# Optimization experiments

Hardware: AMD Instinct MI355X
Metric: run time of the kernel (lower is better)

## Reference

```python
import jax, jax.numpy as jnp
import numpy as np

TREE_DEPTH = 8
N_INTERNAL = 2 ** TREE_DEPTH - 1   # 255
N_LEAVES = 2 ** TREE_DEPTH         # 256
N_CLASSES = 100
N_TREES = 16
BATCH = 8192
D_FEAT = 1024
TEMPERATURE = 1.0


def setup_inputs() -> dict:
    key = jax.random.key(0)
    k1, k2, k3, k4, k5 = jax.random.split(key, 5)
    x = jax.random.normal(k1, (BATCH, D_FEAT), dtype=jnp.float32)
    # scale weights ~1/sqrt(D) so split logits are O(1) (avoids sigmoid saturation)
    split_weights = jax.random.normal(k2, (N_TREES, N_INTERNAL, D_FEAT), dtype=jnp.float32) / np.sqrt(D_FEAT)
    split_bias = jax.random.normal(k3, (N_TREES, N_INTERNAL), dtype=jnp.float32)
    leaf_logits = jax.random.normal(k4, (N_TREES, N_LEAVES, N_CLASSES), dtype=jnp.float32)
    tree_weights = jax.random.normal(k5, (N_TREES,), dtype=jnp.float32)
    return {"x": x, "split_weights": split_weights, "split_bias": split_bias,
            "leaf_logits": leaf_logits, "tree_weights": tree_weights}


def reference(x, split_weights, split_bias, leaf_logits, tree_weights):
    # All internal-node split logits in one contraction: [T, B, N_INTERNAL]
    logits = jnp.einsum('bd,tnd->tbn', x, split_weights) + split_bias[:, None, :]
    split_prob = jax.nn.sigmoid(logits / TEMPERATURE)  # P(go right) per heap node
    T, B = split_prob.shape[0], split_prob.shape[1]
    # Level-order path products. Heap layout: level d occupies nodes [2^d-1, 2^(d+1)-2].
    # Child j of a node splits into (left=2j, right=2j+1) at next level -> interleave.
    mu = jnp.ones((T, B, 1), dtype=x.dtype)
    for d in range(TREE_DEPTH):
        start = 2 ** d - 1
        p = split_prob[:, :, start:start + 2 ** d]          # [T, B, 2^d]
        mu = jnp.stack([mu * (1.0 - p), mu * p], axis=-1)   # left, right
        mu = mu.reshape(T, B, 2 ** (d + 1))
    # mu: [T, B, N_LEAVES] leaf reach probabilities, ordering matches leaf_idx
    leaf_dist = jax.nn.softmax(leaf_logits, axis=-1)        # [T, L, C]
    per_tree = jnp.einsum('tbl,tlc->tbc', mu, leaf_dist)    # [T, B, C]
    w = jax.nn.softmax(tree_weights, axis=0)[:, None, None]
    return (per_tree * w).sum(axis=0)                       # [B, C]
```

## Files before the change

### kernel.cpp

```cpp
#include <hip/hip_runtime.h>
#include <hip/hip_fp16.h>

typedef _Float16 f16;
typedef _Float16 f16x4 __attribute__((ext_vector_type(4)));
typedef _Float16 f16x8 __attribute__((ext_vector_type(8)));
typedef float    f32x4 __attribute__((ext_vector_type(4)));

constexpr int TREES = 16;
constexpr int NNODE = 255;
constexpr int NCLS  = 100;
constexpr int NCPAD = 112;
constexpr int NB    = 8192;
constexpr int DF    = 1024;
constexpr int KTOT  = TREES * 256;

constexpr size_t XH_OFF = 0;
constexpr size_t WH_OFF = XH_OFF + (size_t)NB * DF;
constexpr size_t SD_OFF = WH_OFF + (size_t)TREES * 256 * DF;
constexpr size_t BP_OFF = SD_OFF + (size_t)NCPAD * KTOT;
constexpr size_t PT_OFF_F = (BP_OFF + 8192) / 2;

#define WAIT_VMCNT(n) asm volatile("s_waitcnt vmcnt(" #n ")" ::: "memory")
#define WAIT_LGKM0()  asm volatile("s_waitcnt lgkmcnt(0)" ::: "memory")
__device__ __forceinline__ void BAR() {
  asm volatile("" ::: "memory");
  __builtin_amdgcn_s_barrier();
  asm volatile("" ::: "memory");
}

__device__ __forceinline__ void gload_lds16(const f16* g, f16* l) {
  __builtin_amdgcn_global_load_lds(
      (const __attribute__((address_space(1))) void*)g,
      (__attribute__((address_space(3))) void*)l, 16, 0, 0);
}

__global__ void prep_all_k(const float* __restrict__ x, const float* __restrict__ w,
                           const float* __restrict__ ll, const float* __restrict__ twin,
                           const float* __restrict__ sb,
                           f16* __restrict__ xh, f16* __restrict__ wh,
                           f16* __restrict__ sdt, float* __restrict__ bp) {
  int bid = blockIdx.x;
  if (bid < 4096) {
    int i = bid * 256 + threadIdx.x;
    const float4* s = (const float4*)x + (size_t)i * 2;
    float4 u = s[0], v = s[1];
    f16x8 h = {(f16)u.x, (f16)u.y, (f16)u.z, (f16)u.w,
               (f16)v.x, (f16)v.y, (f16)v.z, (f16)v.w};
    *((f16x8*)xh + i) = h;
  } else if (bid < 6144) {
    int i = (bid - 4096) * 256 + threadIdx.x;
    int flat = i * 8;
    int t = flat >> 18;
    int r = (flat >> 10) & 255;
    int k = flat & 1023;
    f16x8 h;
    if (r < NNODE) {
      const float4* s = (const float4*)(w + ((size_t)(t * NNODE + r) * DF + k));
      float4 u = s[0], v = s[1];
      h = (f16x8){(f16)u.x, (f16)u.y, (f16)u.z, (f16)u.w,
                  (f16)v.x, (f16)v.y, (f16)v.z, (f16)v.w};
    } else {
      h = (f16x8){(f16)0.f, (f16)0.f, (f16)0.f, (f16)0.f,
                  (f16)0.f, (f16)0.f, (f16)0.f, (f16)0.f};
    }
    *((f16x8*)wh + i) = h;
  } else {
    int wv   = threadIdx.x >> 6;
    int lane = threadIdx.x & 63;
    int id   = (bid - 6144) * 4 + wv;
    int t    = id >> 8;
    int node = id & 255;

    float wm = -1e30f;
#pragma unroll
    for (int i = 0; i < 16; ++i) wm = fmaxf(wm, twin[i]);
    float wsum = 0.f;
#pragma unroll
    for (int i = 0; i < 16; ++i) wsum += __expf(twin[i] - wm);
    float wt = __expf(twin[t] - wm) / wsum;

    const float* rowp = ll + (size_t)id * NCLS;
    float v1 = rowp[lane];
    bool has2 = (lane + 64) < NCLS;
    float v2 = has2 ? rowp[lane + 64] : -1e30f;
    float mx = fmaxf(v1, v2);
#pragma unroll
    for (int m = 32; m; m >>= 1) mx = fmaxf(mx, __shfl_xor(mx, m, 64));
    float e1 = __expf(v1 - mx);
    float e2 = has2 ? __expf(v2 - mx) : 0.f;
    float ss = e1 + e2;
#pragma unroll
    for (int m = 32; m; m >>= 1) ss += __shfl_xor(ss, m, 64);
    float inv = wt / ss;

    sdt[(size_t)lane * KTOT + id] = (f16)(e1 * inv);
    if (lane + 64 < NCPAD)
      sdt[(size_t)(lane + 64) * KTOT + id] = has2 ? (f16)(e2 * inv) : (f16)0.f;
    if (lane == 0) bp[id] = (node < NNODE) ? sb[(size_t)t * NNODE + node] : 0.f;
  }
}

__global__ __launch_bounds__(512, 2) void tree_gemm1(
    const f16* __restrict__ xh, const f16* __restrict__ wh,
    const float* __restrict__ biasp, const f16* __restrict__ sdt,
    float* __restrict__ ptree) {
  __shared__ f16 smem[81920];
  char* smb = (char*)smem;

  const int tid  = threadIdx.x;
  const int lane = tid & 63;
  const int wid  = tid >> 6;
  const int l15  = lane & 15;
  const int lq   = lane >> 4;
  const int wrow = (wid >> 2) * 128;
  const int wcol = (wid & 3) * 64;

  int bid  = blockIdx.x;
  int xcd  = bid & 7;
  int idx  = bid >> 3;
  int t    = (xcd & 1) * 8 + (idx & 7);
  int brow = (xcd >> 1) * 8 + (idx >> 3);

  const f16* xsrc = xh + (size_t)brow * 256 * DF;
  const f16* wsrc = wh + (size_t)t * 256 * DF;

  auto stage2 = [&](int kt, int b, int pair) {
    f16* base = smem + b * 16384 + pair * 8192;
    const f16* src = (pair == 0 ? xsrc : wsrc) + kt * 32;
#pragma unroll
    for (int ch = 0; ch < 2; ++ch) {
      int u = ch * 512 + tid;
      int r = u >> 2;
      int ci = (u & 3) ^ (r & 3);
      gload_lds16(src + (size_t)r * DF + ci * 8, base + u * 8);
    }
  };

  f32x4 acc[8][4];
#pragma unroll
  for (int m = 0; m < 8; ++m)
#pragma unroll
    for (int n = 0; n < 4; ++n) acc[m][n] = (f32x4){0.f, 0.f, 0.f, 0.f};

  stage2(0, 0, 0); stage2(0, 0, 1);
  stage2(1, 1, 0); stage2(1, 1, 1);
  WAIT_VMCNT(4);
  BAR();

  for (int kt = 0; kt < 32; ++kt) {
    const char* Ab = smb + (kt % 3) * 32768;
    const char* Bb = Ab + 16384;
    const int nb3 = (kt + 2) % 3;
    f16x8 af[4], bf[4], ag[4];

#pragma unroll
    for (int m = 0; m < 4; ++m) {
      int r = wrow + m * 16 + l15;
      af[m] = *(const f16x8*)(Ab + ((r * 64 + lq * 16) ^ ((r & 3) << 4)));
    }
#pragma unroll
    for (int n = 0; n < 4; ++n) {
      int r = wcol + n * 16 + l15;
      bf[n] = *(const f16x8*)(Bb + ((r * 64 + lq * 16) ^ ((r & 3) << 4)));
    }
    if (kt < 30) stage2(kt + 2, nb3, 0);
    BAR();
    WAIT_LGKM0();
    __builtin_amdgcn_sched_barrier(0);
    __builtin_amdgcn_s_setprio(1);
#pragma unroll
    for (int m = 0; m < 4; ++m)
#pragma unroll
      for (int n = 0; n < 4; ++n)
        acc[m][n] = __builtin_amdgcn_mfma_f32_16x16x32_f16(bf[n], af[m], acc[m][n], 0, 0, 0);
    __builtin_amdgcn_s_setprio(0);
    __builtin_amdgcn_sched_barrier(0);

#pragma unroll
    for (int m = 0; m < 4; ++m) {
      int r = wrow + 64 + m * 16 + l15;
      ag[m] = *(const f16x8*)(Ab + ((r * 64 + lq * 16) ^ ((r & 3) << 4)));
    }
    if (kt < 30) stage2(kt + 2, nb3, 1);
    BAR();
    WAIT_LGKM0();
    __builtin_amdgcn_sched_barrier(0);
    __builtin_amdgcn_s_setprio(1);
#pragma unroll
    for (int m = 0; m < 4; ++m)
#pragma unroll
      for (int n = 0; n < 4; ++n)
        acc[m + 4][n] = __builtin_amdgcn_mfma_f32_16x16x32_f16(bf[n], ag[m], acc[m + 4][n], 0, 0, 0);
    __builtin_amdgcn_s_setprio(0);
    __builtin_amdgcn_sched_barrier(0);

    if (kt < 30)       { WAIT_VMCNT(4); BAR(); }
    else if (kt == 30) { WAIT_VMCNT(0); BAR(); }
  }

  char* Sb = smb;
  char* Ub = smb + 32768;
  char* Pb = smb + 98304;

  auto stage_sdt = [&](int c0, int nrows) {
    int nch = nrows * 32;
    for (int q = tid; q < nch; q += 512) {
      int rr = q >> 5;
      int jj = q & 31;
      gload_lds16(sdt + (size_t)(c0 + rr) * KTOT + t * 256 + ((jj * 8) ^ ((rr & 7) << 3)),
                  smem + q * 8);
    }
  };
  stage_sdt(0, 64);

  f16x4 ph[8][4];
#pragma unroll
  for (int m = 0; m < 8; ++m) {
#pragma unroll
    for (int n = 0; n < 4; ++n) {
      int col = wcol + n * 16 + lq * 4;
      float4 b4 = *(const float4*)(biasp + t * 256 + col);
#pragma unroll
      for (int reg = 0; reg < 4; ++reg) {
        float bv = (reg == 0) ? b4.x : (reg == 1) ? b4.y : (reg == 2) ? b4.z : b4.w;
        float z = acc[m][n][reg] + bv;
        ph[m][n][reg] = (f16)__builtin_amdgcn_rcpf(1.f + __expf(-z));
      }
    }
  }

  for (int h = 0; h < 2; ++h) {
    if ((wid >> 2) == h) {
#pragma unroll
      for (int m = 0; m < 8; ++m) {
#pragma unroll
        for (int n = 0; n < 4; ++n) {
          int r = m * 16 + l15;
          int nodeb = (wcol + n * 16 + lq * 4) * 2;
          *(f16x4*)(Pb + ((r * 512 + nodeb) ^ ((r & 7) << 4))) = ph[m][n];
        }
      }
    }
    __syncthreads();

    {
      int r = tid >> 2;
      int c = tid & 3;
      auto PRs = [&](int node) -> float {
        return (float)*(const f16*)(Pb + ((r * 512 + node * 2) ^ ((r & 7) << 4)));
      };
      auto V8 = [&](int node) -> f16x8 {
        return *(const f16x8*)(Pb + ((r * 512 + node * 2) ^ ((r & 7) << 4)));
      };
      float p0 = PRs(0);
      float p1 = PRs(1 + (c >> 1));
      float pr = ((c >> 1) ? p0 : 1.f - p0) * ((c & 1) ? p1 : 1.f - p1);
      float p2 = PRs(3 + c);
      float cur[64];
      {
        float mp = pr * p2;
        cur[1] = mp; cur[0] = pr - mp;
      }
      {
        float q0 = PRs(7 + 2 * c), q1 = PRs(8 + 2 * c);
        float m1 = cur[1], mp1 = m1 * q1;
        cur[3] = mp1; cur[2] = m1 - mp1;
        float m0 = cur[0], mp0 = m0 * q0;
        cur[1] = mp0; cur[0] = m0 - mp0;
      }
      {
        float q[4];
        q[0] = PRs(15 + 4 * c);
        f16x4 v = *(const f16x4*)(Pb + ((r * 512 + (16 + 4 * c) * 2) ^ ((r & 7) << 4)));
        q[1] = (float)v[0]; q[2] = (float)v[1]; q[3] = (float)v[2];
#pragma unroll
        for (int i = 3; i >= 0; --i) {
          float mv = cur[i], mp = mv * q[i];
          cur[2 * i + 1] = mp; cur[2 * i] = mv - mp;
        }
      }
      {
        float q[8];
        q[0] = PRs(31 + 8 * c);
        f16x8 v = V8(32 + 8 * c);
#pragma unroll
        for (int j = 0; j < 7; ++j) q[j + 1] = (float)v[j];
#pragma unroll
        for (int i = 7; i >= 0; --i) {
          float mv = cur[i], mp = mv * q[i];
          cur[2 * i + 1] = mp; cur[2 * i] = mv - mp;
        }
      }
      {
        float q[16];
        q[0] = PRs(63 + 16 * c);
        f16x8 v0 = V8(64 + 16 * c), v1 = V8(72 + 16 * c);
#pragma unroll
        for (int j = 0; j < 8; ++j) q[j + 1] = (float)v0[j];
#pragma unroll
        for (int j = 0; j < 7; ++j) q[j + 9] = (float)v1[j];
#pragma unroll
        for (int i = 15; i >= 0; --i) {
          float mv = cur[i], mp = mv * q[i];
          cur[2 * i + 1] = mp; cur[2 * i] = mv - mp;
        }
      }
      {
        float q[32];
        q[0] = PRs(127 + 32 * c);
        f16x8 v0 = V8(128 + 32 * c), v1 = V8(136 + 32 * c);
        f16x8 v2 = V8(144 + 32 * c), v3 = V8(152 + 32 * c);
#pragma unroll
        for (int j = 0; j < 8; ++j) q[j + 1]  = (float)v0[j];
#pragma unroll
        for (int j = 0; j < 8; ++j) q[j + 9]  = (float)v1[j];
#pragma unroll
        for (int j = 0; j < 8; ++j) q[j + 17] = (float)v2[j];
#pragma unroll
        for (int j = 0; j < 7; ++j) q[j + 25] = (float)v3[j];
#pragma unroll
        for (int i = 31; i >= 0; --i) {
          float mv = cur[i], mp = mv * q[i];
          cur[2 * i + 1] = mp; cur[2 * i] = mv - mp;
        }
      }
#pragma unroll
      for (int g = 0; g < 8; ++g) {
        f16x8 v;
#pragma unroll
        for (int jj = 0; jj < 8; ++jj) v[jj] = (f16)cur[g * 8 + jj];
        *(f16x8*)(Ub + ((r * 512 + c * 128 + g * 16) ^ ((r & 7) << 4))) = v;
      }
    }
    WAIT_VMCNT(0);
    __syncthreads();

    f32x4 acc2[7];
#pragma unroll
    for (int n = 0; n < 7; ++n) acc2[n] = (f32x4){0.f, 0.f, 0.f, 0.f};
    int arow = wid * 16 + l15;

#pragma unroll
    for (int n = 0; n < 4; ++n) {
#pragma unroll
      for (int s = 0; s < 8; ++s) {
        f16x8 a = *(const f16x8*)(Ub + ((arow * 512 + s * 64 + lq * 16) ^ ((arow & 7) << 4)));
        int br = n * 16 + l15;
        f16x8 b = *(const f16x8*)(Sb + ((br * 512 + s * 64 + lq * 16) ^ ((br & 7) << 4)));
        acc2[n] = __builtin_amdgcn_mfma_f32_16x16x32_f16(a, b, acc2[n], 0, 0, 0);
      }
    }
    __syncthreads();
    stage_sdt(64, 48);
    WAIT_VMCNT(0);
    __syncthreads();
#pragma unroll
    for (int n = 4; n < 7; ++n) {
#pragma unroll
      for (int s = 0; s < 8; ++s) {
        f16x8 a = *(const f16x8*)(Ub + ((arow * 512 + s * 64 + lq * 16) ^ ((arow & 7) << 4)));
        int br = (n - 4) * 16 + l15;
        f16x8 b = *(const f16x8*)(Sb + ((br * 512 + s * 64 + lq * 16) ^ ((br & 7) << 4)));
        acc2[n] = __builtin_amdgcn_mfma_f32_16x16x32_f16(a, b, acc2[n], 0, 0, 0);
      }
    }

    float* pt = ptree + ((size_t)t * NB + brow * 256 + h * 128) * NCLS;
#pragma unroll
    for (int n = 0; n < 7; ++n) {
      int col = n * 16 + l15;
      if (col < NCLS) {
#pragma unroll
        for (int reg = 0; reg < 4; ++reg) {
          int r = wid * 16 + lq * 4 + reg;
          pt[(size_t)r * NCLS + col] = acc2[n][reg];
        }
      }
    }
    if (h == 0) {
      __syncthreads();
      stage_sdt(0, 64);
    }
  }
}

__global__ void reduce_k(const float* __restrict__ pt, float* __restrict__ out) {
  int i = blockIdx.x * 256 + threadIdx.x;
  constexpr size_t STRIDE4 = (size_t)NB * NCLS / 4;
  const float4* p = (const float4*)pt + i;
  float4 s = p[0];
#pragma unroll
  for (int t = 1; t < TREES; ++t) {
    float4 v = p[t * STRIDE4];
    s.x += v.x; s.y += v.y; s.z += v.z; s.w += v.w;
  }
  ((float4*)out)[i] = s;
}

extern "C" void kernel_launch(void* const* d_in, const int* in_sizes, int n_in,
                              void* d_out, int out_size, void* d_ws, size_t ws_size,
                              hipStream_t stream) {
  const float* x  = (const float*)d_in[0];
  const float* sw = (const float*)d_in[1];
  const float* sb = (const float*)d_in[2];
  const float* ll = (const float*)d_in[3];
  const float* tw = (const float*)d_in[4];
  float* out = (float*)d_out;

  f16* ws  = (f16*)d_ws;
  f16* xh  = ws + XH_OFF;
  f16* wh  = ws + WH_OFF;
  f16* sdt = ws + SD_OFF;
  float* biasp = (float*)(ws + BP_OFF);
  float* ptree = (float*)d_ws + PT_OFF_F;

  prep_all_k<<<7168, 256, 0, stream>>>(x, sw, ll, tw, sb, xh, wh, sdt, biasp);
  tree_gemm1<<<512, 512, 0, stream>>>(xh, wh, biasp, sdt, ptree);
  reduce_k<<<(NB * NCLS / 4) / 256, 256, 0, stream>>>(ptree, out);
}
```

Before: 205.9 us.

## Restructure GEMM main loop into double-buffered 64-wide K steps with prefetched sdt

The split-logit GEMM main loop moves from a 3-stage ring of 32-wide K tiles to double-buffered 64-wide K tiles. Each tile is split into two K-halves and loaded in quarter chunks interleaved with the MFMA phases. The LDS swizzle changes to an 8-row XOR pattern with a permuted row mapping, meant to cut bank conflicts. The sdt leaf-table staging is folded into the last iteration so its load overlaps compute. The trade-off is more barriers per iteration and tighter vmcnt bookkeeping, which adds risk of races and stalls.

```diff
diff --git a/kernel.cpp b/kernel.cpp
--- a/kernel.cpp
+++ b/kernel.cpp
@@ -21,7 +21,6 @@
 constexpr size_t PT_OFF_F = (BP_OFF + 8192) / 2;
 
 #define WAIT_VMCNT(n) asm volatile("s_waitcnt vmcnt(" #n ")" ::: "memory")
-#define WAIT_LGKM0()  asm volatile("s_waitcnt lgkmcnt(0)" ::: "memory")
 __device__ __forceinline__ void BAR() {
   asm volatile("" ::: "memory");
   __builtin_amdgcn_s_barrier();
@@ -124,49 +123,58 @@
   const f16* xsrc = xh + (size_t)brow * 256 * DF;
   const f16* wsrc = wh + (size_t)t * 256 * DF;
 
-  auto stage2 = [&](int kt, int b, int pair) {
-    f16* base = smem + b * 16384 + pair * 8192;
-    const f16* src = (pair == 0 ? xsrc : wsrc) + kt * 32;
+  auto stage_ht = [&](int kt, int cb, int op, int kh) {
+    const f16* srcb = (op == 0 ? xsrc : wsrc) + kt * 64 + kh * 32;
+    f16* dstb = smem + cb * 32768 + op * 16384 + kh * 8192;
 #pragma unroll
     for (int ch = 0; ch < 2; ++ch) {
-      int u = ch * 512 + tid;
-      int r = u >> 2;
-      int ci = (u & 3) ^ (r & 3);
-      gload_lds16(src + (size_t)r * DF + ci * 8, base + u * 8);
+      int u  = ch * 512 + tid;
+      int r0 = ((u >> 2) ^ (u >> 4)) & 1;
+      int r1 = (u >> 3) & 1;
+      int r2 = (u >> 4) & 1;
+      int r  = r0 | (r1 << 1) | (r2 << 2) | ((u >> 5) << 3);
+      int cs = ((u ^ r0) & 1) | ((((u >> 1) ^ r1) & 1) << 1);
+      gload_lds16(srcb + (size_t)r * DF + cs * 8, dstb + u * 8);
     }
   };
 
+  auto sdt_stage2 = [&](int c) {
+#pragma unroll
+    for (int ch = 0; ch < 2; ++ch) {
+      int q  = c * 1024 + ch * 512 + tid;
+      int rr = q >> 5;
+      int jj = q & 31;
+      gload_lds16(sdt + (size_t)rr * KTOT + t * 256 + ((jj * 8) ^ ((rr & 7) << 3)),
+                  smem + q * 8);
+    }
+  };
+
+  auto ldop = [&](const char* half_base, int row) -> f16x8 {
+    return *(const f16x8*)(half_base + ((row * 64 + lq * 16) ^ ((row & 7) << 4)));
+  };
+
   f32x4 acc[8][4];
 #pragma unroll
   for (int m = 0; m < 8; ++m)
 #pragma unroll
     for (int n = 0; n < 4; ++n) acc[m][n] = (f32x4){0.f, 0.f, 0.f, 0.f};
 
-  stage2(0, 0, 0); stage2(0, 0, 1);
-  stage2(1, 1, 0); stage2(1, 1, 1);
-  WAIT_VMCNT(4);
-  BAR();
-
-  for (int kt = 0; kt < 32; ++kt) {
-    const char* Ab = smb + (kt % 3) * 32768;
-    const char* Bb = Ab + 16384;
-    const int nb3 = (kt + 2) % 3;
-    f16x8 af[4], bf[4], ag[4];
-
-#pragma unroll
-    for (int m = 0; m < 4; ++m) {
-      int r = wrow + m * 16 + l15;
-      af[m] = *(const f16x8*)(Ab + ((r * 64 + lq * 16) ^ ((r & 3) << 4)));
-    }
-#pragma unroll
-    for (int n = 0; n < 4; ++n) {
-      int r = wcol + n * 16 + l15;
-      bf[n] = *(const f16x8*)(Bb + ((r * 64 + lq * 16) ^ ((r & 3) << 4)));
-    }
-    if (kt < 30) stage2(kt + 2, nb3, 0);
-    BAR();
-    WAIT_LGKM0();
-    __builtin_amdgcn_sched_barrier(0);
+  stage_ht(0, 0, 0, 0); stage_ht(0, 0, 1, 0);
+  stage_ht(0, 0, 0, 1); stage_ht(0, 0, 1, 1);
+
+  for (int kt = 0; kt < 16; ++kt) {
+    const char* Acur = smb + (kt & 1) * 65536;
+    const char* Bcur = Acur + 32768;
+    const int cn = (kt & 1) ^ 1;
+    f16x8 af[4], bf[4];
+
+    if (kt < 15) stage_ht(kt + 1, cn, 0, 0); else sdt_stage2(0);
+    WAIT_VMCNT(6);
+    BAR();
+#pragma unroll
+    for (int m = 0; m < 4; ++m) af[m] = ldop(Acur, wrow + m * 16 + l15);
+#pragma unroll
+    for (int n = 0; n < 4; ++n) bf[n] = ldop(Bcur, wcol + n * 16 + l15);
     __builtin_amdgcn_s_setprio(1);
 #pragma unroll
     for (int m = 0; m < 4; ++m)
@@ -174,28 +182,51 @@
       for (int n = 0; n < 4; ++n)
         acc[m][n] = __builtin_amdgcn_mfma_f32_16x16x32_f16(bf[n], af[m], acc[m][n], 0, 0, 0);
     __builtin_amdgcn_s_setprio(0);
-    __builtin_amdgcn_sched_barrier(0);
-
-#pragma unroll
-    for (int m = 0; m < 4; ++m) {
-      int r = wrow + 64 + m * 16 + l15;
-      ag[m] = *(const f16x8*)(Ab + ((r * 64 + lq * 16) ^ ((r & 3) << 4)));
-    }
-    if (kt < 30) stage2(kt + 2, nb3, 1);
-    BAR();
-    WAIT_LGKM0();
+    BAR();
+
+#pragma unroll
+    for (int m = 0; m < 4; ++m) af[m] = ldop(Acur, wrow + 64 + m * 16 + l15);
+    if (kt < 15) stage_ht(kt + 1, cn, 1, 0);
+    BAR();
     __builtin_amdgcn_sched_barrier(0);
     __builtin_amdgcn_s_setprio(1);
 #pragma unroll
     for (int m = 0; m < 4; ++m)
 #pragma unroll
       for (int n = 0; n < 4; ++n)
-        acc[m + 4][n] = __builtin_amdgcn_mfma_f32_16x16x32_f16(bf[n], ag[m], acc[m + 4][n], 0, 0, 0);
+        acc[m + 4][n] = __builtin_amdgcn_mfma_f32_16x16x32_f16(bf[n], af[m], acc[m + 4][n], 0, 0, 0);
     __builtin_amdgcn_s_setprio(0);
+    BAR();
+
+    if (kt < 15) { stage_ht(kt + 1, cn, 0, 1); WAIT_VMCNT(6); }
+    else         { sdt_stage2(1);              WAIT_VMCNT(4); }
+    BAR();
+#pragma unroll
+    for (int m = 0; m < 4; ++m) af[m] = ldop(Acur + 16384, wrow + m * 16 + l15);
+#pragma unroll
+    for (int n = 0; n < 4; ++n) bf[n] = ldop(Bcur + 16384, wcol + n * 16 + l15);
+    __builtin_amdgcn_s_setprio(1);
+#pragma unroll
+    for (int m = 0; m < 4; ++m)
+#pragma unroll
+      for (int n = 0; n < 4; ++n)
+        acc[m][n] = __builtin_amdgcn_mfma_f32_16x16x32_f16(bf[n], af[m], acc[m][n], 0, 0, 0);
+    __builtin_amdgcn_s_setprio(0);
+    BAR();
+
+#pragma unroll
+    for (int m = 0; m < 4; ++m) af[m] = ldop(Acur + 16384, wrow + 64 + m * 16 + l15);
+    if (kt < 15) stage_ht(kt + 1, cn, 1, 1);
+    BAR();
     __builtin_amdgcn_sched_barrier(0);
-
-    if (kt < 30)       { WAIT_VMCNT(4); BAR(); }
-    else if (kt == 30) { WAIT_VMCNT(0); BAR(); }
+    __builtin_amdgcn_s_setprio(1);
+#pragma unroll
+    for (int m = 0; m < 4; ++m)
+#pragma unroll
+      for (int n = 0; n < 4; ++n)
+        acc[m + 4][n] = __builtin_amdgcn_mfma_f32_16x16x32_f16(bf[n], af[m], acc[m + 4][n], 0, 0, 0);
+    __builtin_amdgcn_s_setprio(0);
+    BAR();
   }
 
   char* Sb = smb;
@@ -211,7 +242,6 @@
                   smem + q * 8);
     }
   };
-  stage_sdt(0, 64);
 
   f16x4 ph[8][4];
 #pragma unroll
```

Result: faster. 199.1 us (-3.3%).
